# Optimization experiments

Hardware: AMD Instinct MI355X
Metric: run time of the kernel (lower is better)

## Reference

```python
import jax, jax.numpy as jnp
import numpy as np

B, H, W, C = 8, 64, 64, 256
C8 = C // 8  # query/key channels


def setup_inputs() -> dict:
    key = jax.random.key(0)
    ks = jax.random.split(key, 8)
    s = 0.02  # init scale for weights
    return {
        "x": jax.random.normal(ks[0], (B, H, W, C), dtype=jnp.float32),
        "Wq": jax.random.normal(ks[1], (C, C8), dtype=jnp.float32) * s,
        "bq": jnp.zeros((C8,), dtype=jnp.float32),
        "Wk": jax.random.normal(ks[2], (C, C8), dtype=jnp.float32) * s,
        "bk": jnp.zeros((C8,), dtype=jnp.float32),
        "Wv": jax.random.normal(ks[3], (C, C), dtype=jnp.float32) * s,
        "bv": jnp.zeros((C,), dtype=jnp.float32),
        "gamma": jnp.full((1,), 0.5, dtype=jnp.float32),
    }


def reference(x, Wq, bq, Wk, bk, Wv, bv, gamma):
    Bn, Hn, Wn, Cn = x.shape
    N = Hn * Wn
    xf = x.reshape(Bn, N, Cn)            # flatten spatial dims: [B, N, C]
    # 1x1 convs == per-pixel dense projections over channels
    q = xf @ Wq + bq                     # [B, N, C//8]
    k = xf @ Wk + bk                     # [B, N, C//8]
    v = xf @ Wv + bv                     # [B, N, C]
    # energy[b,i,j] = k_i . q_j  (matches tf.matmul(key, query, transpose_b=True))
    energy = jnp.einsum('bic,bjc->bij', k, q)   # [B, N, N]
    attn = jax.nn.softmax(energy, axis=-1)      # softmax over last axis
    # out_i = sum_j attn[i,j] * v_j  (intended SAGAN aggregation in NHWC layout)
    out = jnp.einsum('bij,bjc->bic', attn, v)   # [B, N, C]
    out = out.reshape(Bn, Hn, Wn, Cn)
    return gamma * out + x
```

## Files before the change

kernel.cpp:

```cpp
#include <hip/hip_runtime.h>

typedef __attribute__((ext_vector_type(8))) short short8;
typedef __attribute__((ext_vector_type(4))) float f32x4;
typedef __attribute__((ext_vector_type(16))) float f32x16;
typedef __attribute__((ext_vector_type(2))) unsigned int u32x2;
typedef __attribute__((ext_vector_type(4))) unsigned int u32x4;
typedef unsigned short u16;
typedef unsigned int u32;

#define MFMA16(a, b, c) __builtin_amdgcn_mfma_f32_16x16x32_bf16((a), (b), (c), 0, 0, 0)
#define MFMA32(a, b, c) __builtin_amdgcn_mfma_f32_32x32x16_bf16((a), (b), (c), 0, 0, 0)

#define BATCH 8
#define NTOK 4096
#define CDIM 256
#define CQK 32
#define LOG2E 1.4426950408889634f

__device__ __forceinline__ u16 f2bf(float f) {
  u32 u = __float_as_uint(f);
  return (u16)((u + 0x7FFFu + ((u >> 16) & 1u)) >> 16);
}
__device__ __forceinline__ u32 pack2(float a, float b) {
  const u32 ua = __float_as_uint(a) + 0x8000u;
  const u32 ub = __float_as_uint(b) + 0x8000u;
#if __has_builtin(__builtin_amdgcn_perm)
  return __builtin_amdgcn_perm(ub, ua, 0x07060302u);
#else
  return (ua >> 16) | (ub & 0xFFFF0000u);
#endif
}
__device__ __forceinline__ float fexp2(float x) {
#if __has_builtin(__builtin_amdgcn_exp2f)
  return __builtin_amdgcn_exp2f(x);
#else
  return exp2f(x);
#endif
}

__global__ void k_prep(const float* __restrict__ Wq, const float* __restrict__ bq,
                       const float* __restrict__ Wk, const float* __restrict__ bk,
                       const float* __restrict__ Wv, const float* __restrict__ bv,
                       u16* __restrict__ wtf, float* __restrict__ bias) {
  const int f = blockIdx.x;
  const int L = threadIdx.x;
  const int ct = f >> 3, ks = f & 7;
  const int o = ct * 16 + (L & 15);
  const int ch = ks * 32 + (L >> 4) * 8;
  short8 v8;
#pragma unroll
  for (int jj = 0; jj < 8; jj++) {
    const int c = ch + jj;
    float v;
    if (o < 32)       v = Wq[c * CQK + o];
    else if (o < 64)  v = Wk[c * CQK + (o - 32)];
    else              v = Wv[c * CDIM + (o - 64)];
    v8[jj] = (short)f2bf(v);
  }
  *(short8*)(wtf + (size_t)f * 512 + L * 8) = v8;
  if (f == 0) {
    for (int i = L; i < 320; i += 64) {
      if (i < 32)      bias[i] = bq[i];
      else if (i < 64) bias[i] = bk[i - 32];
      else             bias[i] = bv[i - 64];
    }
  }
}

__global__ __launch_bounds__(256, 2) void k_proj(
    const float* __restrict__ x, const u16* __restrict__ wtf,
    const float* __restrict__ bias,
    u16* __restrict__ q_ws, u16* __restrict__ k_ws, u16* __restrict__ vt_ws) {
  __shared__ u16 x_lds[64 * 264];
  __shared__ u16 vt_t[64 * 76];
  const int m0 = blockIdx.x * 64;
  const int tid = threadIdx.x;
  const int w = tid >> 6, L = tid & 63;
  const int lr = L & 15, q4 = L >> 4;

  short8 wfA[5], wfB[5];
#pragma unroll
  for (int j = 0; j < 5; j++)
    wfA[j] = *(const short8*)(wtf + ((size_t)((j * 4 + w) * 8 + 0)) * 512 + L * 8);

#pragma unroll
  for (int ii = 0; ii < 8; ii++) {
    const int e = (tid + 256 * ii) * 8;
    const int row = e >> 8, col = e & 255;
    const float* src = x + (size_t)(m0 + row) * CDIM + col;
    f32x4 a = *(const f32x4*)src;
    f32x4 b4 = *(const f32x4*)(src + 4);
    u32x4 pk;
    pk[0] = pack2(a[0], a[1]);
    pk[1] = pack2(a[2], a[3]);
    pk[2] = pack2(b4[0], b4[1]);
    pk[3] = pack2(b4[2], b4[3]);
    *(u32x4*)&x_lds[row * 264 + col] = pk;
  }
  __syncthreads();

  f32x4 acc[4][5];
#pragma unroll
  for (int rg = 0; rg < 4; rg++)
#pragma unroll
    for (int j = 0; j < 5; j++) acc[rg][j] = (f32x4){0.f, 0.f, 0.f, 0.f};

#pragma unroll
  for (int ks = 0; ks < 8; ks++) {
    if (ks < 7) {
#pragma unroll
      for (int j = 0; j < 5; j++) {
        short8 v = *(const short8*)(wtf +
            ((size_t)((j * 4 + w) * 8 + ks + 1)) * 512 + L * 8);
        if (ks & 1) wfA[j] = v; else wfB[j] = v;
      }
    }
#pragma unroll
    for (int rg = 0; rg < 4; rg++) {
      short8 a = *(const short8*)&x_lds[(rg * 16 + lr) * 264 + ks * 32 + q4 * 8];
#pragma unroll
      for (int j = 0; j < 5; j++)
        acc[rg][j] = MFMA16(a, (ks & 1) ? wfB[j] : wfA[j], acc[rg][j]);
    }
  }

  {
    const float bb = bias[w * 16 + lr];
#pragma unroll
    for (int rg = 0; rg < 4; rg++)
#pragma unroll
      for (int r = 0; r < 4; r++) {
        const int row = m0 + rg * 16 + q4 * 4 + r;
        float v = acc[rg][0][r] + bb;
        if (w < 2) q_ws[(size_t)row * CQK + w * 16 + lr] = f2bf(v);
        else       k_ws[(size_t)row * CQK + (w - 2) * 16 + lr] = f2bf(v * LOG2E);
      }
  }
  const int b = m0 >> 12, nt = (m0 & 4095) >> 6;
  const int c_l = w * 16 + lr;
#pragma unroll
  for (int cg = 0; cg < 4; cg++) {
    __syncthreads();
    const int j = cg + 1;
    const float bb = bias[(4 + cg * 4 + w) * 16 + lr];
#pragma unroll
    for (int rg = 0; rg < 4; rg++) {
      u32x2 pk;
      pk[0] = pack2(acc[rg][j][0] + bb, acc[rg][j][1] + bb);
      pk[1] = pack2(acc[rg][j][2] + bb, acc[rg][j][3] + bb);
      *(u32x2*)&vt_t[c_l * 76 + rg * 16 + q4 * 4] = pk;
    }
    __syncthreads();
#pragma unroll
    for (int i = 0; i < 2; i++) {
      const int gch = tid + 256 * i;
      const int fid = gch >> 6;
      const int lane = gch & 63;
      const int jt = fid >> 2, kh = (fid >> 1) & 1, ct2 = fid & 1;
      const int cc = ct2 * 32 + (lane & 31);
      const int n0 = jt * 32 + kh * 16 + (lane >> 5) * 4;
      u32x2 va = *(const u32x2*)&vt_t[cc * 76 + n0];
      u32x2 vb2 = *(const u32x2*)&vt_t[cc * 76 + n0 + 8];
      u32x4 vv = {va[0], va[1], vb2[0], vb2[1]};
      *(short8*)(vt_ws +
          ((((size_t)(b * 64 + nt) * 4 + cg) * 8 + fid) * 512) + lane * 8) =
          __builtin_bit_cast(short8, vv);
    }
  }
}

__global__ __launch_bounds__(256, 2) void k_attn(
    const float* __restrict__ x, const u16* __restrict__ q_ws,
    const u16* __restrict__ k_ws, const u16* __restrict__ vt_ws,
    const float* __restrict__ gamma, float* __restrict__ out) {
  __shared__ float lp4[4][64];

  const int bid = blockIdx.x;
  const int b = bid & 7;
  const int i0 = (bid >> 3) * 64;
  const int tid = threadIdx.x;
  const int w = tid >> 6, L = tid & 63;
  const int L31 = L & 31, Lhi = L >> 5;

  const u16* kb = k_ws + ((size_t)(b * NTOK + i0 + L31)) * CQK + Lhi * 8;
  const u16* qb = q_ws + ((size_t)(b * NTOK) + L31) * CQK + Lhi * 8;
  const u16* vb = vt_ws + ((size_t)b << 20) + w * 4096 + (size_t)L * 8;

  f32x16 z16;
#pragma unroll
  for (int e = 0; e < 16; e++) z16[e] = 0.f;
  f32x16 o00 = z16, o01 = z16, o10 = z16, o11 = z16;
  float ls0 = 0.f, ls1 = 0.f;

  short8 vV0 = *(const short8*)(vb + 0 * 512);
  short8 vV1 = *(const short8*)(vb + 1 * 512);
  short8 vV2 = *(const short8*)(vb + 2 * 512);
  short8 vV3 = *(const short8*)(vb + 3 * 512);
  short8 vV4 = *(const short8*)(vb + 4 * 512);
  short8 vV5 = *(const short8*)(vb + 5 * 512);
  short8 vV6 = *(const short8*)(vb + 6 * 512);
  short8 vV7 = *(const short8*)(vb + 7 * 512);
  const short8 kf00 = *(const short8*)(kb);
  const short8 kf01 = *(const short8*)(kb + 16);
  const short8 kf10 = *(const short8*)(kb + 32 * CQK);
  const short8 kf11 = *(const short8*)(kb + 32 * CQK + 16);
  short8 q00 = *(const short8*)(qb);
  short8 q01 = *(const short8*)(qb + 16);
  short8 q10 = *(const short8*)(qb + 32 * CQK);
  short8 q11 = *(const short8*)(qb + 32 * CQK + 16);

#define EPPV(SV, V0, V1, V2, V3, OA, OB, LS)                                   \
  do {                                                                         \
    float e0 = fexp2((SV)[0]), e1 = fexp2((SV)[1]);                            \
    float e2 = fexp2((SV)[2]), e3 = fexp2((SV)[3]);                            \
    float e4 = fexp2((SV)[4]), e5 = fexp2((SV)[5]);                            \
    float e6 = fexp2((SV)[6]), e7 = fexp2((SV)[7]);                            \
    float e8 = fexp2((SV)[8]), e9 = fexp2((SV)[9]);                            \
    float e10 = fexp2((SV)[10]), e11 = fexp2((SV)[11]);                        \
    float e12 = fexp2((SV)[12]), e13 = fexp2((SV)[13]);                        \
    float e14 = fexp2((SV)[14]), e15 = fexp2((SV)[15]);                        \
    LS += ((((e0 + e1) + (e2 + e3)) + ((e4 + e5) + (e6 + e7))) +               \
           (((e8 + e9) + (e10 + e11)) + ((e12 + e13) + (e14 + e15))));         \
    u32x4 pA = {pack2(e0, e1), pack2(e2, e3), pack2(e4, e5), pack2(e6, e7)};   \
    u32x4 pB = {pack2(e8, e9), pack2(e10, e11), pack2(e12, e13),               \
                pack2(e14, e15)};                                              \
    const short8 a0 = __builtin_bit_cast(short8, pA);                          \
    const short8 a1 = __builtin_bit_cast(short8, pB);                          \
    OA = MFMA32(a0, V0, OA);                                                   \
    OB = MFMA32(a0, V1, OB);                                                   \
    OA = MFMA32(a1, V2, OA);                                                   \
    OB = MFMA32(a1, V3, OB);                                                   \
  } while (0)

#define UNIT(QA, QB, KA, KB, V0, V1, V2, V3, OA, OB, LS)                       \
  do {                                                                         \
    f32x16 sv_ = MFMA32(QA, KA, z16);                                          \
    sv_ = MFMA32(QB, KB, sv_);                                                 \
    EPPV(sv_, V0, V1, V2, V3, OA, OB, LS);                                     \
  } while (0)

  for (int t = 0; t < 64; ++t) {
    const size_t vn = (size_t)(t + 1) * 16384;
    UNIT(q00, q01, kf00, kf01, vV0, vV1, vV2, vV3, o00, o01, ls0);
    UNIT(q10, q11, kf00, kf01, vV4, vV5, vV6, vV7, o00, o01, ls0);
    UNIT(q00, q01, kf10, kf11, vV0, vV1, vV2, vV3, o10, o11, ls1);
    vV0 = *(const short8*)(vb + vn + 0 * 512);
    vV1 = *(const short8*)(vb + vn + 1 * 512);
    vV2 = *(const short8*)(vb + vn + 2 * 512);
    vV3 = *(const short8*)(vb + vn + 3 * 512);
    f32x16 svz = MFMA32(q10, kf10, z16);
    svz = MFMA32(q11, kf11, svz);
    {
      const size_t qo = (size_t)(t + 1) * 64 * CQK;
      q00 = *(const short8*)(qb + qo);
      q01 = *(const short8*)(qb + qo + 16);
      q10 = *(const short8*)(qb + qo + 32 * CQK);
      q11 = *(const short8*)(qb + qo + 32 * CQK + 16);
    }
    EPPV(svz, vV4, vV5, vV6, vV7, o10, o11, ls1);
    vV4 = *(const short8*)(vb + vn + 4 * 512);
    vV5 = *(const short8*)(vb + vn + 5 * 512);
    vV6 = *(const short8*)(vb + vn + 6 * 512);
    vV7 = *(const short8*)(vb + vn + 7 * 512);
  }
#undef UNIT
#undef EPPV

  ls0 += __shfl_xor(ls0, 32);
  ls1 += __shfl_xor(ls1, 32);
  if (L < 32) {
    lp4[w][L] = 1.0f / ls0;
    lp4[w][32 + L] = 1.0f / ls1;
  }
  asm volatile("s_waitcnt lgkmcnt(0)" ::: "memory");

  float linv[2][16];
#pragma unroll
  for (int ih = 0; ih < 2; ih++)
#pragma unroll
    for (int rg = 0; rg < 16; rg++)
      linv[ih][rg] = lp4[w][ih * 32 + (rg & 3) + 8 * (rg >> 2) + 4 * Lhi];

  const float g = gamma[0];
#define STO(OV, IH, CT2)                                                       \
  _Pragma("unroll")                                                            \
  for (int rg = 0; rg < 16; rg++) {                                            \
    const int i = i0 + (IH) * 32 + (rg & 3) + 8 * (rg >> 2) + 4 * Lhi;         \
    const int c = w * 64 + (CT2) * 32 + L31;                                   \
    const size_t idx = ((size_t)(b * NTOK + i)) * CDIM + c;                    \
    out[idx] = g * (OV[rg] * linv[IH][rg]) + x[idx];                           \
  }
  STO(o00, 0, 0)
  STO(o01, 0, 1)
  STO(o10, 1, 0)
  STO(o11, 1, 1)
#undef STO
}

extern "C" void kernel_launch(void* const* d_in, const int* in_sizes, int n_in,
                              void* d_out, int out_size, void* d_ws, size_t ws_size,
                              hipStream_t stream) {
  const float* x  = (const float*)d_in[0];
  const float* Wq = (const float*)d_in[1];
  const float* bq = (const float*)d_in[2];
  const float* Wk = (const float*)d_in[3];
  const float* bk = (const float*)d_in[4];
  const float* Wv = (const float*)d_in[5];
  const float* bv = (const float*)d_in[6];
  const float* gamma = (const float*)d_in[7];
  float* out = (float*)d_out;

  char* ws = (char*)d_ws;
  u16* q_ws  = (u16*)(ws);
  u16* k_ws  = (u16*)(ws + (2u << 20));
  u16* vt_ws = (u16*)(ws + (4u << 20));
  u16* wtf   = (u16*)(ws + (20u << 20));
  float* bias = (float*)(ws + (20u << 20) + (256u << 10));

  k_prep<<<160, 64, 0, stream>>>(Wq, bq, Wk, bk, Wv, bv, wtf, bias);
  k_proj<<<512, 256, 0, stream>>>(x, wtf, bias, q_ws, k_ws, vt_ws);
  k_attn<<<512, 256, 0, stream>>>(x, q_ws, k_ws, vt_ws, gamma, out);
}
```

Measured before the change: 214.3 us.

## Repartition attention waves to 32 rows by 128 channels instead of 64 by 64

Each wave in the attention kernel now owns 32 query rows and 128 output channels, where before it owned 64 rows and 64 channels. The QK score tile is computed once per wave per 64-key step instead of four times, which removes duplicated exp and pack work. In exchange each wave loads twice as many V fragments (16 short8 registers), which raises register pressure and V read traffic per wave. The softmax normalizer bookkeeping is reduced to a single row sum accordingly.

```diff
diff --git a/kernel.cpp b/kernel.cpp
--- a/kernel.cpp
+++ b/kernel.cpp
@@ -173,43 +173,51 @@
     const float* __restrict__ x, const u16* __restrict__ q_ws,
     const u16* __restrict__ k_ws, const u16* __restrict__ vt_ws,
     const float* __restrict__ gamma, float* __restrict__ out) {
-  __shared__ float lp4[4][64];
+  __shared__ float lp4[4][32];
 
   const int bid = blockIdx.x;
   const int b = bid & 7;
-  const int i0 = (bid >> 3) * 64;
   const int tid = threadIdx.x;
   const int w = tid >> 6, L = tid & 63;
   const int L31 = L & 31, Lhi = L >> 5;
+  const int i0 = (bid >> 3) * 64 + (w >> 1) * 32;
+  const int chh = w & 1;
 
   const u16* kb = k_ws + ((size_t)(b * NTOK + i0 + L31)) * CQK + Lhi * 8;
+  const short8 kf0 = *(const short8*)(kb);
+  const short8 kf1 = *(const short8*)(kb + 16);
   const u16* qb = q_ws + ((size_t)(b * NTOK) + L31) * CQK + Lhi * 8;
-  const u16* vb = vt_ws + ((size_t)b << 20) + w * 4096 + (size_t)L * 8;
+  const u16* vb = vt_ws + ((size_t)b << 20) + (size_t)(chh * 2) * 4096 +
+                  (size_t)L * 8;
 
   f32x16 z16;
 #pragma unroll
   for (int e = 0; e < 16; e++) z16[e] = 0.f;
   f32x16 o00 = z16, o01 = z16, o10 = z16, o11 = z16;
-  float ls0 = 0.f, ls1 = 0.f;
-
-  short8 vV0 = *(const short8*)(vb + 0 * 512);
-  short8 vV1 = *(const short8*)(vb + 1 * 512);
-  short8 vV2 = *(const short8*)(vb + 2 * 512);
-  short8 vV3 = *(const short8*)(vb + 3 * 512);
-  short8 vV4 = *(const short8*)(vb + 4 * 512);
-  short8 vV5 = *(const short8*)(vb + 5 * 512);
-  short8 vV6 = *(const short8*)(vb + 6 * 512);
-  short8 vV7 = *(const short8*)(vb + 7 * 512);
-  const short8 kf00 = *(const short8*)(kb);
-  const short8 kf01 = *(const short8*)(kb + 16);
-  const short8 kf10 = *(const short8*)(kb + 32 * CQK);
-  const short8 kf11 = *(const short8*)(kb + 32 * CQK + 16);
+  float ls = 0.f;
+
+  short8 u0 = *(const short8*)(vb + 0);
+  short8 u1 = *(const short8*)(vb + 512);
+  short8 u2 = *(const short8*)(vb + 1024);
+  short8 u3 = *(const short8*)(vb + 1536);
+  short8 u4 = *(const short8*)(vb + 4096);
+  short8 u5 = *(const short8*)(vb + 4096 + 512);
+  short8 u6 = *(const short8*)(vb + 4096 + 1024);
+  short8 u7 = *(const short8*)(vb + 4096 + 1536);
+  short8 v0 = *(const short8*)(vb + 2048);
+  short8 v1 = *(const short8*)(vb + 2048 + 512);
+  short8 v2 = *(const short8*)(vb + 2048 + 1024);
+  short8 v3 = *(const short8*)(vb + 2048 + 1536);
+  short8 v4 = *(const short8*)(vb + 4096 + 2048);
+  short8 v5 = *(const short8*)(vb + 4096 + 2048 + 512);
+  short8 v6 = *(const short8*)(vb + 4096 + 2048 + 1024);
+  short8 v7 = *(const short8*)(vb + 4096 + 2048 + 1536);
   short8 q00 = *(const short8*)(qb);
   short8 q01 = *(const short8*)(qb + 16);
   short8 q10 = *(const short8*)(qb + 32 * CQK);
   short8 q11 = *(const short8*)(qb + 32 * CQK + 16);
 
-#define EPPV(SV, V0, V1, V2, V3, OA, OB, LS)                                   \
+#define EPPV(SV, W0, W1, W2, W3, W4, W5, W6, W7)                               \
   do {                                                                         \
     float e0 = fexp2((SV)[0]), e1 = fexp2((SV)[1]);                            \
     float e2 = fexp2((SV)[2]), e3 = fexp2((SV)[3]);                            \
@@ -219,37 +227,38 @@
     float e10 = fexp2((SV)[10]), e11 = fexp2((SV)[11]);                        \
     float e12 = fexp2((SV)[12]), e13 = fexp2((SV)[13]);                        \
     float e14 = fexp2((SV)[14]), e15 = fexp2((SV)[15]);                        \
-    LS += ((((e0 + e1) + (e2 + e3)) + ((e4 + e5) + (e6 + e7))) +               \
+    ls += ((((e0 + e1) + (e2 + e3)) + ((e4 + e5) + (e6 + e7))) +               \
            (((e8 + e9) + (e10 + e11)) + ((e12 + e13) + (e14 + e15))));         \
     u32x4 pA = {pack2(e0, e1), pack2(e2, e3), pack2(e4, e5), pack2(e6, e7)};   \
     u32x4 pB = {pack2(e8, e9), pack2(e10, e11), pack2(e12, e13),               \
                 pack2(e14, e15)};                                              \
     const short8 a0 = __builtin_bit_cast(short8, pA);                          \
     const short8 a1 = __builtin_bit_cast(short8, pB);                          \
-    OA = MFMA32(a0, V0, OA);                                                   \
-    OB = MFMA32(a0, V1, OB);                                                   \
-    OA = MFMA32(a1, V2, OA);                                                   \
-    OB = MFMA32(a1, V3, OB);                                                   \
+    o00 = MFMA32(a0, W0, o00);                                                 \
+    o01 = MFMA32(a0, W1, o01);                                                 \
+    o10 = MFMA32(a0, W4, o10);                                                 \
+    o11 = MFMA32(a0, W5, o11);                                                 \
+    o00 = MFMA32(a1, W2, o00);                                                 \
+    o01 = MFMA32(a1, W3, o01);                                                 \
+    o10 = MFMA32(a1, W6, o10);                                                 \
+    o11 = MFMA32(a1, W7, o11);                                                 \
   } while (0)
 
-#define UNIT(QA, QB, KA, KB, V0, V1, V2, V3, OA, OB, LS)                       \
-  do {                                                                         \
-    f32x16 sv_ = MFMA32(QA, KA, z16);                                          \
-    sv_ = MFMA32(QB, KB, sv_);                                                 \
-    EPPV(sv_, V0, V1, V2, V3, OA, OB, LS);                                     \
-  } while (0)
-
   for (int t = 0; t < 64; ++t) {
-    const size_t vn = (size_t)(t + 1) * 16384;
-    UNIT(q00, q01, kf00, kf01, vV0, vV1, vV2, vV3, o00, o01, ls0);
-    UNIT(q10, q11, kf00, kf01, vV4, vV5, vV6, vV7, o00, o01, ls0);
-    UNIT(q00, q01, kf10, kf11, vV0, vV1, vV2, vV3, o10, o11, ls1);
-    vV0 = *(const short8*)(vb + vn + 0 * 512);
-    vV1 = *(const short8*)(vb + vn + 1 * 512);
-    vV2 = *(const short8*)(vb + vn + 2 * 512);
-    vV3 = *(const short8*)(vb + vn + 3 * 512);
-    f32x16 svz = MFMA32(q10, kf10, z16);
-    svz = MFMA32(q11, kf11, svz);
+    const u16* vn = vb + (size_t)(t + 1) * 16384;
+    f32x16 sv0 = MFMA32(q00, kf0, z16);
+    sv0 = MFMA32(q01, kf1, sv0);
+    EPPV(sv0, u0, u1, u2, u3, u4, u5, u6, u7);
+    u0 = *(const short8*)(vn + 0);
+    u1 = *(const short8*)(vn + 512);
+    u2 = *(const short8*)(vn + 1024);
+    u3 = *(const short8*)(vn + 1536);
+    u4 = *(const short8*)(vn + 4096);
+    u5 = *(const short8*)(vn + 4096 + 512);
+    u6 = *(const short8*)(vn + 4096 + 1024);
+    u7 = *(const short8*)(vn + 4096 + 1536);
+    f32x16 sv1 = MFMA32(q10, kf0, z16);
+    sv1 = MFMA32(q11, kf1, sv1);
     {
       const size_t qo = (size_t)(t + 1) * 64 * CQK;
       q00 = *(const short8*)(qb + qo);
@@ -257,38 +266,35 @@
       q10 = *(const short8*)(qb + qo + 32 * CQK);
       q11 = *(const short8*)(qb + qo + 32 * CQK + 16);
     }
-    EPPV(svz, vV4, vV5, vV6, vV7, o10, o11, ls1);
-    vV4 = *(const short8*)(vb + vn + 4 * 512);
-    vV5 = *(const short8*)(vb + vn + 5 * 512);
-    vV6 = *(const short8*)(vb + vn + 6 * 512);
-    vV7 = *(const short8*)(vb + vn + 7 * 512);
-  }
-#undef UNIT
+    EPPV(sv1, v0, v1, v2, v3, v4, v5, v6, v7);
+    v0 = *(const short8*)(vn + 2048);
+    v1 = *(const short8*)(vn + 2048 + 512);
+    v2 = *(const short8*)(vn + 2048 + 1024);
+    v3 = *(const short8*)(vn + 2048 + 1536);
+    v4 = *(const short8*)(vn + 4096 + 2048);
+    v5 = *(const short8*)(vn + 4096 + 2048 + 512);
+    v6 = *(const short8*)(vn + 4096 + 2048 + 1024);
+    v7 = *(const short8*)(vn + 4096 + 2048 + 1536);
+  }
 #undef EPPV
 
-  ls0 += __shfl_xor(ls0, 32);
-  ls1 += __shfl_xor(ls1, 32);
-  if (L < 32) {
-    lp4[w][L] = 1.0f / ls0;
-    lp4[w][32 + L] = 1.0f / ls1;
-  }
+  ls += __shfl_xor(ls, 32);
+  if (L < 32) lp4[w][L] = 1.0f / ls;
   asm volatile("s_waitcnt lgkmcnt(0)" ::: "memory");
 
-  float linv[2][16];
-#pragma unroll
-  for (int ih = 0; ih < 2; ih++)
-#pragma unroll
-    for (int rg = 0; rg < 16; rg++)
-      linv[ih][rg] = lp4[w][ih * 32 + (rg & 3) + 8 * (rg >> 2) + 4 * Lhi];
+  float linv[16];
+#pragma unroll
+  for (int rg = 0; rg < 16; rg++)
+    linv[rg] = lp4[w][(rg & 3) + 8 * (rg >> 2) + 4 * Lhi];
 
   const float g = gamma[0];
-#define STO(OV, IH, CT2)                                                       \
+#define STO(OV, CB2, CT2)                                                      \
   _Pragma("unroll")                                                            \
   for (int rg = 0; rg < 16; rg++) {                                            \
-    const int i = i0 + (IH) * 32 + (rg & 3) + 8 * (rg >> 2) + 4 * Lhi;         \
-    const int c = w * 64 + (CT2) * 32 + L31;                                   \
+    const int i = i0 + (rg & 3) + 8 * (rg >> 2) + 4 * Lhi;                     \
+    const int c = (chh * 2 + (CB2)) * 64 + (CT2) * 32 + L31;                   \
     const size_t idx = ((size_t)(b * NTOK + i)) * CDIM + c;                    \
-    out[idx] = g * (OV[rg] * linv[IH][rg]) + x[idx];                           \
+    out[idx] = g * (OV[rg] * linv[rg]) + x[idx];                               \
   }
   STO(o00, 0, 0)
   STO(o01, 0, 1)
```

Measured after the change: 205.6 us. 1.04x faster.
